# Optimization experiments

Measured on AMD Instinct MI355X. Metric: run time of the kernel, lower is better.

## Reference

```python
import jax, jax.numpy as jnp
import numpy as np

DELTA = 5.0   # weight on positive term
GAMMA = 0.01  # fraction of negatives kept as hard negatives


def setup_inputs() -> dict:
    key = jax.random.key(0)
    k1, k2 = jax.random.split(key)
    m, n = 4096, 16384
    inputs = jax.random.normal(k1, (m, n), dtype=jnp.float32)
    targets = jax.random.randint(k2, (m,), 0, n)
    return {"inputs": inputs, "targets": targets}


def reference(inputs, targets):
    # inputs: [m, n] logits; targets: [m] class indices (one positive per row)
    m, n = inputs.shape
    num_neg = n - 1                      # one positive per row -> n-1 negatives
    k = int(GAMMA * num_neg)             # matches int(self.gamma * neg_logit.size(0))

    # positive logit per row (pos_logit has exactly 1 element, mean == itself)
    pos = jnp.take_along_axis(inputs, targets[:, None], axis=1)[:, 0]  # [m]

    # mask out the positive so top_k selects only negatives
    neg_masked = inputs.at[jnp.arange(m), targets].set(-jnp.inf)       # [m, n]
    hard_neg, _ = jax.lax.top_k(neg_masked, k)                         # [m, k]

    loss_per_row = DELTA * (pos - 1.0) ** 2 + jnp.mean((hard_neg + 1.0) ** 2, axis=1)
    return jnp.mean(loss_per_row)
```

## Files before the change

kernel.cpp:

```cpp
#include <hip/hip_runtime.h>

#define M        4096
#define N        16384
#define K_SEL    163
#define DELTA_W  5.0f
#define NT       256
#define CAPW     512
#define SCALE    4096.0f
#define THRESH   2.0f

typedef float vfloat4 __attribute__((ext_vector_type(4)));

__device__ __forceinline__ unsigned f2key(float x) {
    unsigned u = __float_as_uint(x);
    return u ^ ((unsigned)((int)u >> 31) | 0x80000000u);
}
__device__ __forceinline__ float key2f(unsigned k) {
    unsigned u = k ^ (~(unsigned)((int)k >> 31) | 0x80000000u);
    return __uint_as_float(u);
}
__device__ __forceinline__ void wave_lgkm_wait() {
    asm volatile("s_waitcnt lgkmcnt(0)" ::: "memory");
}

__global__ __launch_bounds__(NT, 4) void fused_row_loss(
    const float* __restrict__ inp, const int* __restrict__ tgt,
    float* __restrict__ row_loss)
{
    __shared__ unsigned hist_all[4][256];
    __shared__ unsigned list_all[4][CAPW];
    const int lane = threadIdx.x & 63;
    const int wv   = threadIdx.x >> 6;
    const int row  = blockIdx.x * 4 + wv;
    unsigned* hist = hist_all[wv];
    unsigned* list = list_all[wv];
    const float* rp = inp + (size_t)row * N;
    const vfloat4* rp4 = reinterpret_cast<const vfloat4*>(rp);
    const int target = tgt[row];

    unsigned long long w0 = 0, w1 = 0, w2 = 0, w3 = 0;
    #pragma unroll
    for (int bb = 0; bb < 4; ++bb) {
        vfloat4 v[16];
        #pragma unroll
        for (int u = 0; u < 16; ++u) v[u] = rp4[(bb * 16 + u) * 64 + lane];
        #pragma unroll
        for (int u = 0; u < 16; ++u) {
            const int it = bb * 16 + u;
            unsigned long long b0 = __ballot(v[u][0] >= THRESH);
            unsigned long long b1 = __ballot(v[u][1] >= THRESH);
            unsigned long long b2 = __ballot(v[u][2] >= THRESH);
            unsigned long long b3 = __ballot(v[u][3] >= THRESH);
            if (lane == it) { w0 = b0; w1 = b1; w2 = b2; w3 = b3; }
        }
    }

    if ((target >> 8) == lane) {
        const int j = target & 3;
        const unsigned long long bit = 1ull << ((target & 255) >> 2);
        if (j == 0) w0 &= ~bit;
        if (j == 1) w1 &= ~bit;
        if (j == 2) w2 &= ~bit;
        if (j == 3) w3 &= ~bit;
    }

    const unsigned myc = (unsigned)(__popcll(w0) + __popcll(w1)
                                  + __popcll(w2) + __popcll(w3));
    unsigned inc = myc;
    #pragma unroll
    for (int off = 1; off < 64; off <<= 1) {
        unsigned t = __shfl_up(inc, off);
        if (lane >= off) inc += t;
    }
    const unsigned C   = __shfl(inc, 63);
    const unsigned pre = inc - myc;

    float loss = 0.0f;
    bool have = false;

    if (C >= K_SEL && C <= CAPW) {
        unsigned pos = pre;
        #pragma unroll
        for (int j = 0; j < 4; ++j) {
            unsigned long long m = (j == 0) ? w0 : (j == 1) ? w1 : (j == 2) ? w2 : w3;
            while (m) {
                const int p = __builtin_ctzll(m); m &= m - 1;
                list[pos++] = (unsigned)(lane * 256 + 4 * p + j);
            }
        }
        wave_lgkm_wait();

        float vals[8];
        #pragma unroll
        for (int it = 0; it < 8; ++it) {
            const unsigned i = lane + it * 64u;
            const unsigned a = (i < C) ? list[i] : 0u;
            vals[it] = rp[a];
        }
        unsigned keys[8];
        #pragma unroll
        for (int it = 0; it < 8; ++it) {
            const unsigned i = lane + it * 64u;
            keys[it] = (i < C) ? f2key(vals[it]) : 0u;
        }

        unsigned mn = 0xFFFFFFFFu, mx = 0u;
        #pragma unroll
        for (int it = 0; it < 8; ++it) {
            const unsigned i = lane + it * 64u;
            if (i < C) { mn = min(mn, keys[it]); mx = max(mx, keys[it]); }
        }
        #pragma unroll
        for (int off = 32; off > 0; off >>= 1) {
            mn = min(mn, (unsigned)__shfl_xor((int)mn, off));
            mx = max(mx, (unsigned)__shfl_xor((int)mx, off));
        }
        const unsigned diff = mn ^ mx;
        const int b0i = (diff == 0u) ? 3 : (__clz(diff) >> 3);
        unsigned prefix = (b0i == 0) ? 0u : (mn >> (32 - 8 * b0i));
        unsigned kr = K_SEL;

        for (int pass = b0i; pass < 4; ++pass) {
            *reinterpret_cast<uint4*>(&hist[lane * 4]) = make_uint4(0, 0, 0, 0);
            wave_lgkm_wait();
            const int shift = 24 - 8 * pass;
            #pragma unroll
            for (int it = 0; it < 8; ++it) {
                unsigned k = keys[it];
                bool mm = (lane + it * 64u < C) &&
                          (pass == 0 || (k >> (shift + 8)) == prefix);
                if (mm) atomicAdd(&hist[(k >> shift) & 0xFFu], 1u);
            }
            wave_lgkm_wait();
            uint4 h = *reinterpret_cast<const uint4*>(&hist[lane * 4]);
            unsigned hb[4] = {h.x, h.y, h.z, h.w};
            unsigned s_local = hb[0] + hb[1] + hb[2] + hb[3];
            unsigned suf = s_local;
            #pragma unroll
            for (int off = 1; off < 64; off <<= 1) {
                unsigned o = __shfl_down(suf, off);
                suf += (lane + off < 64) ? o : 0u;
            }
            unsigned acc_above = suf - s_local;
            int foundc = -1; unsigned f_abv = 0;
            #pragma unroll
            for (int c = 3; c >= 0; --c) {
                unsigned S = acc_above + hb[c];
                if (acc_above < kr && S >= kr) { foundc = c; f_abv = acc_above; }
                acc_above = S;
            }
            bool win = (foundc >= 0);
            unsigned long long bal = __ballot(win);
            int wl = __ffsll((long long)bal) - 1;
            unsigned np = win ? ((prefix << 8) | (unsigned)(lane * 4 + foundc)) : 0u;
            unsigned nk = win ? (kr - f_abv) : 0u;
            prefix = __shfl(np, wl);
            kr     = __shfl(nk, wl);
        }
        const unsigned tkey = prefix, krem = kr;

        int facc = 0;
        #pragma unroll
        for (int it = 0; it < 8; ++it) {
            unsigned k = keys[it];
            if ((lane + it * 64u) < C && k > tkey) {
                float ww = key2f(k) + 1.0f;
                facc += (int)(ww * ww * SCALE + 0.5f);
            }
        }
        #pragma unroll
        for (int off = 32; off > 0; off >>= 1) facc += __shfl_down(facc, off);
        if (lane == 0) {
            float tv    = key2f(tkey) + 1.0f;
            float total = (float)facc * (1.0f / SCALE) + (float)krem * tv * tv;
            float pd    = rp[target] - 1.0f;
            loss = DELTA_W * pd * pd + total * (1.0f / (float)K_SEL);
            have = true;
        }
    } else {
        unsigned prefix = 0u, kr = K_SEL;
        for (int pass = 0; pass < 4; ++pass) {
            *reinterpret_cast<uint4*>(&hist[lane * 4]) = make_uint4(0, 0, 0, 0);
            wave_lgkm_wait();
            const int shift = 24 - 8 * pass;
            for (int it = 0; it < N / 64; ++it) {
                int i = lane + it * 64;
                unsigned k = f2key(rp[i]);
                if (i == target) k = 0u;
                bool mm = (pass == 0) || ((k >> (shift + 8)) == prefix);
                if (mm) atomicAdd(&hist[(k >> shift) & 0xFFu], 1u);
            }
            wave_lgkm_wait();
            uint4 h = *reinterpret_cast<const uint4*>(&hist[lane * 4]);
            unsigned hb[4] = {h.x, h.y, h.z, h.w};
            unsigned s_local = hb[0] + hb[1] + hb[2] + hb[3];
            unsigned suf = s_local;
            #pragma unroll
            for (int off = 1; off < 64; off <<= 1) {
                unsigned o = __shfl_down(suf, off);
                suf += (lane + off < 64) ? o : 0u;
            }
            unsigned acc_above = suf - s_local;
            int foundc = -1; unsigned f_abv = 0;
            #pragma unroll
            for (int c = 3; c >= 0; --c) {
                unsigned S = acc_above + hb[c];
                if (acc_above < kr && S >= kr) { foundc = c; f_abv = acc_above; }
                acc_above = S;
            }
            bool win = (foundc >= 0);
            unsigned long long bal = __ballot(win);
            int wl = __ffsll((long long)bal) - 1;
            unsigned np = win ? ((prefix << 8) | (unsigned)(lane * 4 + foundc)) : 0u;
            unsigned nk = win ? (kr - f_abv) : 0u;
            prefix = __shfl(np, wl);
            kr     = __shfl(nk, wl);
        }
        const unsigned tkey = prefix, krem = kr;

        int facc = 0;
        for (int it = 0; it < N / 64; ++it) {
            int i = lane + it * 64;
            unsigned k = f2key(rp[i]);
            if (i == target) k = 0u;
            if (k > tkey) { float ww = key2f(k) + 1.0f; facc += (int)(ww * ww * SCALE + 0.5f); }
        }
        #pragma unroll
        for (int off = 32; off > 0; off >>= 1) facc += __shfl_down(facc, off);
        if (lane == 0) {
            float tv    = key2f(tkey) + 1.0f;
            float total = (float)facc * (1.0f / SCALE) + (float)krem * tv * tv;
            float pd    = rp[target] - 1.0f;
            loss = DELTA_W * pd * pd + total * (1.0f / (float)K_SEL);
            have = true;
        }
    }

    if (have) row_loss[row] = loss;
}

__global__ __launch_bounds__(256) void final_reduce(
    const float* __restrict__ rl, float* __restrict__ out)
{
    int tid = threadIdx.x;
    float s = 0.0f;
    for (int i = tid; i < M; i += 256) s += rl[i];
    __shared__ float wp[4];
    int lane = tid & 63, wv = tid >> 6;
    #pragma unroll
    for (int off = 32; off > 0; off >>= 1) s += __shfl_down(s, off);
    if (lane == 0) wp[wv] = s;
    __syncthreads();
    if (tid == 0) out[0] = (wp[0] + wp[1] + wp[2] + wp[3]) / (float)M;
}

extern "C" void kernel_launch(void* const* d_in, const int* in_sizes, int n_in,
                              void* d_out, int out_size, void* d_ws, size_t ws_size,
                              hipStream_t stream) {
    const float* inp = (const float*)d_in[0];
    const int*   tgt = (const int*)d_in[1];
    float* out = (float*)d_out;
    float* row_loss = (float*)d_ws;

    fused_row_loss<<<M / 4, NT, 0, stream>>>(inp, tgt, row_loss);
    final_reduce<<<1, 256, 0, stream>>>(row_loss, out);
}
```

Before: 72.24 us.

## Compact candidate keys directly into LDS during the scan instead of re-gathering

The threshold scan now does stream compaction on the fly. Each element's ballot plus mbcnt gives it a slot, and surviving values are written as sortable keys straight into the per-wave LDS list. This replaces the old flow: per-lane bitmasks, a prefix-scan of counts, serial bit extraction of indices, and a second global gather of candidate values. The aim is to remove the scattered global re-reads and the serial ctz loop, at the cost of 256 ballots with per-ballot LDS writes and a smaller load batch (8 vs 16 vec4 loads in flight).

```diff
diff --git a/kernel.cpp b/kernel.cpp
--- a/kernel.cpp
+++ b/kernel.cpp
@@ -38,70 +38,48 @@
     const vfloat4* rp4 = reinterpret_cast<const vfloat4*>(rp);
     const int target = tgt[row];
 
-    unsigned long long w0 = 0, w1 = 0, w2 = 0, w3 = 0;
+    const int it_t = target >> 8;
+    const int l_t  = (target & 255) >> 2;
+    const int j_t  = target & 3;
+
+    unsigned cnt = 0;
     #pragma unroll
-    for (int bb = 0; bb < 4; ++bb) {
-        vfloat4 v[16];
-        #pragma unroll
-        for (int u = 0; u < 16; ++u) v[u] = rp4[(bb * 16 + u) * 64 + lane];
-        #pragma unroll
-        for (int u = 0; u < 16; ++u) {
-            const int it = bb * 16 + u;
-            unsigned long long b0 = __ballot(v[u][0] >= THRESH);
-            unsigned long long b1 = __ballot(v[u][1] >= THRESH);
-            unsigned long long b2 = __ballot(v[u][2] >= THRESH);
-            unsigned long long b3 = __ballot(v[u][3] >= THRESH);
-            if (lane == it) { w0 = b0; w1 = b1; w2 = b2; w3 = b3; }
+    for (int it0 = 0; it0 < 64; it0 += 8) {
+        vfloat4 v[8];
+        #pragma unroll
+        for (int u = 0; u < 8; ++u) v[u] = rp4[(it0 + u) * 64 + lane];
+        #pragma unroll
+        for (int u = 0; u < 8; ++u) {
+            const int it = it0 + u;
+            const bool tgt_here = (it == it_t) && (lane == l_t);
+            #pragma unroll
+            for (int j = 0; j < 4; ++j) {
+                const bool pred = (v[u][j] >= THRESH) && !(tgt_here && j == j_t);
+                const unsigned long long bal = __ballot(pred);
+                if (pred) {
+                    const unsigned rank = __builtin_amdgcn_mbcnt_hi(
+                        (unsigned)(bal >> 32),
+                        __builtin_amdgcn_mbcnt_lo((unsigned)bal, 0u));
+                    const unsigned slot = cnt + rank;
+                    if (slot < CAPW) list[slot] = f2key(v[u][j]);
+                }
+                cnt += (unsigned)__popcll(bal);
+            }
         }
     }
-
-    if ((target >> 8) == lane) {
-        const int j = target & 3;
-        const unsigned long long bit = 1ull << ((target & 255) >> 2);
-        if (j == 0) w0 &= ~bit;
-        if (j == 1) w1 &= ~bit;
-        if (j == 2) w2 &= ~bit;
-        if (j == 3) w3 &= ~bit;
-    }
-
-    const unsigned myc = (unsigned)(__popcll(w0) + __popcll(w1)
-                                  + __popcll(w2) + __popcll(w3));
-    unsigned inc = myc;
-    #pragma unroll
-    for (int off = 1; off < 64; off <<= 1) {
-        unsigned t = __shfl_up(inc, off);
-        if (lane >= off) inc += t;
-    }
-    const unsigned C   = __shfl(inc, 63);
-    const unsigned pre = inc - myc;
+    const unsigned C = cnt;
 
     float loss = 0.0f;
     bool have = false;
 
     if (C >= K_SEL && C <= CAPW) {
-        unsigned pos = pre;
-        #pragma unroll
-        for (int j = 0; j < 4; ++j) {
-            unsigned long long m = (j == 0) ? w0 : (j == 1) ? w1 : (j == 2) ? w2 : w3;
-            while (m) {
-                const int p = __builtin_ctzll(m); m &= m - 1;
-                list[pos++] = (unsigned)(lane * 256 + 4 * p + j);
-            }
-        }
         wave_lgkm_wait();
 
-        float vals[8];
+        unsigned keys[8];
         #pragma unroll
         for (int it = 0; it < 8; ++it) {
             const unsigned i = lane + it * 64u;
-            const unsigned a = (i < C) ? list[i] : 0u;
-            vals[it] = rp[a];
-        }
-        unsigned keys[8];
-        #pragma unroll
-        for (int it = 0; it < 8; ++it) {
-            const unsigned i = lane + it * 64u;
-            keys[it] = (i < C) ? f2key(vals[it]) : 0u;
+            keys[it] = (i < C) ? list[i] : 0u;
         }
 
         unsigned mn = 0xFFFFFFFFu, mx = 0u;
```

After: 62.82 us. 1.15x faster.
